# Kernel optimization log

Measured on AMD Instinct MI355X. Metric: run time of the kernel, lower is better.

Reference implementation:

```python
import jax, jax.numpy as jnp
import numpy as np

DIM = 512
HEADS = 8
EPS = 1e-3  # keras LayerNormalization default epsilon


def setup_inputs() -> dict:
    key = jax.random.key(0)
    ks = jax.random.split(key, 12)
    B, H, W, C = 8, 32, 32, DIM
    s = 0.02
    return {
        "x": jax.random.normal(ks[0], (B, H, W, C), jnp.float32),
        "ln_gamma": jnp.ones((C,), jnp.float32),
        "ln_beta": jnp.zeros((C,), jnp.float32),
        "qkv_d_w": jax.random.normal(ks[1], (C, 3 * C), jnp.float32) * s,
        "qkv_d_b": jnp.zeros((3 * C,), jnp.float32),
        "qkv_s_w": jax.random.normal(ks[2], (C, 3 * C), jnp.float32) * s,
        "qkv_s_b": jnp.zeros((3 * C,), jnp.float32),
        "proj_d_w": jax.random.normal(ks[3], (C, C), jnp.float32) * s,
        "proj_d_b": jnp.zeros((C,), jnp.float32),
        "proj_s_w": jax.random.normal(ks[4], (C, C), jnp.float32) * s,
        "proj_s_b": jnp.zeros((C,), jnp.float32),
        "fusion_weight": jnp.ones((2,), jnp.float32),
    }


def _split_heads(t, B, N):
    # [B, N, C] -> [B, heads, N, head_dim]
    return t.reshape(B, N, HEADS, -1).transpose(0, 2, 1, 3)


def _merge_heads(t, B, N, C):
    # [B, heads, N, head_dim] -> [B, N, C]
    return t.transpose(0, 2, 1, 3).reshape(B, N, C)


def reference(x, ln_gamma, ln_beta, qkv_d_w, qkv_d_b, qkv_s_w, qkv_s_b,
              proj_d_w, proj_d_b, proj_s_w, proj_s_b, fusion_weight):
    B, H, W, C = x.shape
    N = H * W
    scale = (C // HEADS) ** -0.5

    xf = x.reshape(B, N, C)
    mu = jnp.mean(xf, axis=-1, keepdims=True)
    var = jnp.var(xf, axis=-1, keepdims=True)
    xf = (xf - mu) * jax.lax.rsqrt(var + EPS) * ln_gamma + ln_beta

    # dense (softmax) branch
    qkv_d = xf @ qkv_d_w + qkv_d_b
    q_d, k_d, v_d = (
        _split_heads(t, B, N) for t in jnp.split(qkv_d, 3, axis=-1)
    )
    logits_d = jnp.einsum("bhnd,bhmd->bhnm", q_d, k_d) * scale
    out_d = jnp.einsum("bhnm,bhmd->bhnd", jax.nn.softmax(logits_d, axis=-1), v_d)
    out_d = _merge_heads(out_d, B, N, C) @ proj_d_w + proj_d_b

    # sparse (relu^2) branch
    qkv_s = xf @ qkv_s_w + qkv_s_b
    q_s, k_s, v_s = (
        _split_heads(t, B, N) for t in jnp.split(qkv_s, 3, axis=-1)
    )
    rq = jnp.square(jax.nn.relu(q_s))
    rk = jnp.square(jax.nn.relu(k_s))
    logits_s = jnp.einsum("bhnd,bhmd->bhnm", rq, rk) * scale
    out_s = jnp.einsum("bhnm,bhmd->bhnd", logits_s, v_s)
    out_s = _merge_heads(out_s, B, N, C) @ proj_s_w + proj_s_b

    alpha = jax.nn.softmax(fusion_weight)
    out = alpha[0] * out_s + alpha[1] * out_d
    return out.reshape(B, H, W, C)
```

## Files before the change

### kernel.cpp

```cpp
#include <hip/hip_runtime.h>
#include <math.h>

#define M_ROWS   8192
#define CDIM     512
#define QKV_N    1536
#define NTOK     1024
#define HEADS    8
#define HD       64
#define EPS      1e-3f
#define SCALE    0.125f

typedef __attribute__((ext_vector_type(8))) short short8;
typedef __attribute__((ext_vector_type(4))) float f32x4;
typedef unsigned short ushort_t;


__device__ __forceinline__ ushort_t f2bf(float f) {
    union { float f; unsigned int u; } v; v.f = f;
    unsigned int r = v.u + 0x7fffu + ((v.u >> 16) & 1u);
    return (ushort_t)(r >> 16);
}
__device__ __forceinline__ float bf2f(ushort_t u) {
    union { unsigned int u; float f; } v; v.u = ((unsigned int)u) << 16;
    return v.f;
}

__device__ __forceinline__ void get_alpha(const float* __restrict__ fw,
                                          float& a0, float& a1)
{
    const float m  = fmaxf(fw[0], fw[1]);
    const float e0 = __expf(fw[0] - m);
    const float e1 = __expf(fw[1] - m);
    const float inv = 1.0f / (e0 + e1);
    a0 = e0 * inv;
    a1 = e1 * inv;
}


__global__ __launch_bounds__(256) void ln_kernel(const float* __restrict__ x,
                                                 const float* __restrict__ gamma,
                                                 const float* __restrict__ beta,
                                                 ushort_t* __restrict__ xhi,
                                                 ushort_t* __restrict__ xlo)
{
    const int row = blockIdx.x;
    const int t   = threadIdx.x;
    const float2 v = ((const float2*)(x + (size_t)row * CDIM))[t];
    float s  = v.x + v.y;
    float ss = v.x * v.x + v.y * v.y;
#pragma unroll
    for (int off = 32; off > 0; off >>= 1) {
        s  += __shfl_xor(s,  off, 64);
        ss += __shfl_xor(ss, off, 64);
    }
    __shared__ float red[8];
    __shared__ float stats[2];
    const int wid = t >> 6, lane = t & 63;
    if (lane == 0) { red[wid] = s; red[4 + wid] = ss; }
    __syncthreads();
    if (t == 0) {
        const float S  = red[0] + red[1] + red[2] + red[3];
        const float SS = red[4] + red[5] + red[6] + red[7];
        const float mu  = S * (1.0f / CDIM);
        const float var = SS * (1.0f / CDIM) - mu * mu;
        stats[0] = mu;
        stats[1] = rsqrtf(var + EPS);
    }
    __syncthreads();
    const float mu = stats[0], rs = stats[1];
    const float2 gv = ((const float2*)gamma)[t];
    const float2 bv = ((const float2*)beta)[t];
    const float ox = (v.x - mu) * rs * gv.x + bv.x;
    const float oy = (v.y - mu) * rs * gv.y + bv.y;
    ushort2 h2, l2;
    h2.x = f2bf(ox); l2.x = f2bf(ox - bf2f(h2.x));
    h2.y = f2bf(oy); l2.y = f2bf(oy - bf2f(h2.y));
    ((ushort2*)(xhi + (size_t)row * CDIM))[t] = h2;
    ((ushort2*)(xlo + (size_t)row * CDIM))[t] = l2;
}


__global__ __launch_bounds__(256) void tconv_kernel(const float* __restrict__ W,
                                                    ushort_t* __restrict__ hiT,
                                                    ushort_t* __restrict__ loT,
                                                    int N, int ors, int coff)
{
    const int t  = threadIdx.x;
    const int bk = blockIdx.x * 64, bn = blockIdx.y * 64;
    __shared__ float tile[64][65];
#pragma unroll
    for (int i = 0; i < 4; ++i) {
        const int idx = t + i * 256;
        const int kl = idx >> 4, nl = (idx & 15) * 4;
        const float4 v = *(const float4*)(W + (size_t)(bk + kl) * N + bn + nl);
        tile[kl][nl] = v.x; tile[kl][nl + 1] = v.y;
        tile[kl][nl + 2] = v.z; tile[kl][nl + 3] = v.w;
    }
    __syncthreads();
#pragma unroll
    for (int i = 0; i < 2; ++i) {
        const int idx = t + i * 256;
        const int nl = idx >> 3, kc = (idx & 7) * 8;
        short8 hv, lv;
#pragma unroll
        for (int j = 0; j < 8; ++j) {
            const float f = tile[kc + j][nl];
            const ushort_t h = f2bf(f);
            hv[j] = (short)h;
            lv[j] = (short)f2bf(f - bf2f(h));
        }
        const size_t ob = (size_t)(bn + nl) * ors + coff + bk + kc;
        *(short8*)(hiT + ob) = hv;
        if (loT) *(short8*)(loT + ob) = lv;
    }
}


template<int SPLIT, int OUTBF>
__global__ __launch_bounds__(256) void gemm_bf16_mfma(const ushort_t* __restrict__ Ahi,
                                                      const ushort_t* __restrict__ Alo,
                                                      const ushort_t* __restrict__ Bhi,
                                                      const ushort_t* __restrict__ Blo,
                                                      const float* __restrict__ bias,
                                                      float* __restrict__ C,
                                                      ushort_t* __restrict__ Cb,
                                                      int N, int K)
{
    const int t  = threadIdx.x;
    const int l  = t & 63, w = t >> 6;
    const int wr = w >> 1, wc = w & 1;
    const int lr = l & 15, lg = l >> 4;
    const int bm = blockIdx.x * 128, bn = blockIdx.y * 128;

    __shared__ ushort_t As[SPLIT ? 2 : 1][128 * 64];
    __shared__ ushort_t Bs[SPLIT ? 2 : 1][128 * 64];

    f32x4 acc[4][4];
#pragma unroll
    for (int i = 0; i < 4; ++i)
#pragma unroll
        for (int j = 0; j < 4; ++j) acc[i][j] = (f32x4){0.f, 0.f, 0.f, 0.f};

    const int srow0  = t >> 3;
    const int schunk = t & 7;

    for (int kt = 0; kt < K; kt += 64) {
        __syncthreads();
#pragma unroll
        for (int i = 0; i < 4; ++i) {
            const int row = srow0 + i * 32;
            const int cs  = ((schunk ^ (row & 7)) * 8);
            const size_t ga = (size_t)(bm + row) * K + kt + schunk * 8;
            const size_t gb = (size_t)(bn + row) * K + kt + schunk * 8;
            *(short8*)(&As[0][row * 64 + cs]) = *(const short8*)(Ahi + ga);
            *(short8*)(&Bs[0][row * 64 + cs]) = *(const short8*)(Bhi + gb);
            if (SPLIT) {
                *(short8*)(&As[1][row * 64 + cs]) = *(const short8*)(Alo + ga);
                *(short8*)(&Bs[1][row * 64 + cs]) = *(const short8*)(Blo + gb);
            }
        }
        __syncthreads();
#pragma unroll
        for (int ks = 0; ks < 2; ++ks) {
            short8 ah[4], bh[4], al[4], bl[4];
#pragma unroll
            for (int mf = 0; mf < 4; ++mf) {
                const int row = wr * 64 + mf * 16 + lr;
                const int cs  = (((ks * 4 + lg) ^ (row & 7)) * 8);
                ah[mf] = *(const short8*)(&As[0][row * 64 + cs]);
                if (SPLIT) al[mf] = *(const short8*)(&As[1][row * 64 + cs]);
            }
#pragma unroll
            for (int nf = 0; nf < 4; ++nf) {
                const int row = wc * 64 + nf * 16 + lr;
                const int cs  = (((ks * 4 + lg) ^ (row & 7)) * 8);
                bh[nf] = *(const short8*)(&Bs[0][row * 64 + cs]);
                if (SPLIT) bl[nf] = *(const short8*)(&Bs[1][row * 64 + cs]);
            }
#pragma unroll
            for (int mf = 0; mf < 4; ++mf)
#pragma unroll
                for (int nf = 0; nf < 4; ++nf) {
                    acc[mf][nf] = __builtin_amdgcn_mfma_f32_16x16x32_bf16(ah[mf], bh[nf], acc[mf][nf], 0, 0, 0);
                    if (SPLIT) {
                        acc[mf][nf] = __builtin_amdgcn_mfma_f32_16x16x32_bf16(al[mf], bh[nf], acc[mf][nf], 0, 0, 0);
                        acc[mf][nf] = __builtin_amdgcn_mfma_f32_16x16x32_bf16(ah[mf], bl[nf], acc[mf][nf], 0, 0, 0);
                    }
                }
        }
    }
    float bv[4];
#pragma unroll
    for (int nf = 0; nf < 4; ++nf) bv[nf] = bias[bn + wc * 64 + nf * 16 + lr];
#pragma unroll
    for (int mf = 0; mf < 4; ++mf)
#pragma unroll
        for (int r = 0; r < 4; ++r) {
            const int row = bm + wr * 64 + mf * 16 + lg * 4 + r;
            if (OUTBF) {
                ushort_t* cp = Cb + (size_t)row * N + bn + wc * 64;
#pragma unroll
                for (int nf = 0; nf < 4; ++nf)
                    cp[nf * 16 + lr] = f2bf(acc[mf][nf][r] + bv[nf]);
            } else {
                float* cp = C + (size_t)row * N + bn + wc * 64;
#pragma unroll
                for (int nf = 0; nf < 4; ++nf)
                    cp[nf * 16 + lr] = acc[mf][nf][r] + bv[nf];
            }
        }
}


__global__ __launch_bounds__(256) void vt_kernel(const ushort_t* __restrict__ qkvd_bf,
                                                 ushort_t* __restrict__ vtg)
{
    const int t  = threadIdx.x;
    const int bh = blockIdx.x, nt = blockIdx.y;
    const int b  = bh >> 3, h = bh & 7;
    __shared__ ushort_t tile[64 * 72];
    const int row = t >> 2, c16 = (t & 3) * 16;
    const size_t src = (size_t)(b * NTOK + nt * 64 + row) * QKV_N + 2 * CDIM + h * HD + c16;
    *(short8*)(tile + row * 72 + c16)     = *(const short8*)(qkvd_bf + src);
    *(short8*)(tile + row * 72 + c16 + 8) = *(const short8*)(qkvd_bf + src + 8);
    __syncthreads();
    const int d = t >> 2, tc = (t & 3) * 16;
    short8 o0, o1;
#pragma unroll
    for (int i = 0; i < 8; ++i) {
        o0[i] = (short)tile[(tc + i) * 72 + d];
        o1[i] = (short)tile[(tc + 8 + i) * 72 + d];
    }
    const size_t dst = ((size_t)bh * 64 + d) * NTOK + nt * 64 + tc;
    *(short8*)(vtg + dst)     = o0;
    *(short8*)(vtg + dst + 8) = o1;
}


__global__ __launch_bounds__(256) void attn_dense_mfma(const ushort_t* __restrict__ qkvd_bf,
                                                       const ushort_t* __restrict__ vtg,
                                                       const float* __restrict__ fw,
                                                       ushort_t* __restrict__ athi,
                                                       ushort_t* __restrict__ atlo)
{
    const int t  = threadIdx.x;
    const int l  = t & 63;
    const int w  = t >> 6;
    const int lr = l & 15;
    const int lg = l >> 4;

    const int blk = blockIdx.x;
    const int xcd = blk & 7;
    const int ixl = blk >> 3;
    const int bh  = ((ixl >> 4) << 3) + xcd;
    const int qt  = ixl & 15;
    const int b   = bh >> 3, h = bh & 7;

    __shared__ ushort_t Qs[64 * 72];
    __shared__ ushort_t Ks[64 * 72];
    __shared__ ushort_t Vs[64 * 72];
    __shared__ ushort_t Ps[64 * 72];

    const int srow = t >> 2, sc = (t & 3) * 16;

    {
        const size_t src = (size_t)(b * NTOK + qt * 64 + srow) * QKV_N + h * HD + sc;
        *(short8*)(Qs + srow * 72 + sc)     = *(const short8*)(qkvd_bf + src);
        *(short8*)(Qs + srow * 72 + sc + 8) = *(const short8*)(qkvd_bf + src + 8);
    }
    __syncthreads();

    const short8 aQ0 = *(const short8*)(Qs + (w * 16 + lr) * 72 + lg * 8);
    const short8 aQ1 = *(const short8*)(Qs + (w * 16 + lr) * 72 + 32 + lg * 8);

    f32x4 oacc[4];
#pragma unroll
    for (int i = 0; i < 4; ++i) oacc[i] = (f32x4){0.f, 0.f, 0.f, 0.f};
    float lsum[4] = {0.f, 0.f, 0.f, 0.f};

    for (int kt2 = 0; kt2 < 16; ++kt2) {
        __syncthreads();
        {
            const size_t ksrc = (size_t)(b * NTOK + kt2 * 64 + srow) * QKV_N + CDIM + h * HD + sc;
            *(short8*)(Ks + srow * 72 + sc)     = *(const short8*)(qkvd_bf + ksrc);
            *(short8*)(Ks + srow * 72 + sc + 8) = *(const short8*)(qkvd_bf + ksrc + 8);
            const size_t vsrc = ((size_t)bh * 64 + srow) * NTOK + kt2 * 64 + sc;
            *(short8*)(Vs + srow * 72 + sc)     = *(const short8*)(vtg + vsrc);
            *(short8*)(Vs + srow * 72 + sc + 8) = *(const short8*)(vtg + vsrc + 8);
        }
        __syncthreads();

        f32x4 s[4];
#pragma unroll
        for (int nf = 0; nf < 4; ++nf) {
            const short8 b0 = *(const short8*)(Ks + (nf * 16 + lr) * 72 + lg * 8);
            const short8 b1 = *(const short8*)(Ks + (nf * 16 + lr) * 72 + 32 + lg * 8);
            f32x4 z = {0.f, 0.f, 0.f, 0.f};
            z = __builtin_amdgcn_mfma_f32_16x16x32_bf16(aQ0, b0, z, 0, 0, 0);
            z = __builtin_amdgcn_mfma_f32_16x16x32_bf16(aQ1, b1, z, 0, 0, 0);
            s[nf] = z;
        }

#pragma unroll
        for (int nf = 0; nf < 4; ++nf) {
#pragma unroll
            for (int r = 0; r < 4; ++r) {
                const float p = __expf(s[nf][r] * SCALE);
                lsum[r] += p;
                Ps[(w * 16 + lg * 4 + r) * 72 + nf * 16 + lr] = f2bf(p);
            }
        }
        __syncthreads();

        const short8 aP0 = *(const short8*)(Ps + (w * 16 + lr) * 72 + lg * 8);
        const short8 aP1 = *(const short8*)(Ps + (w * 16 + lr) * 72 + 32 + lg * 8);
#pragma unroll
        for (int nfd = 0; nfd < 4; ++nfd) {
            const short8 b0 = *(const short8*)(Vs + (nfd * 16 + lr) * 72 + lg * 8);
            const short8 b1 = *(const short8*)(Vs + (nfd * 16 + lr) * 72 + 32 + lg * 8);
            oacc[nfd] = __builtin_amdgcn_mfma_f32_16x16x32_bf16(aP0, b0, oacc[nfd], 0, 0, 0);
            oacc[nfd] = __builtin_amdgcn_mfma_f32_16x16x32_bf16(aP1, b1, oacc[nfd], 0, 0, 0);
        }
    }

#pragma unroll
    for (int r = 0; r < 4; ++r) {
        lsum[r] += __shfl_xor(lsum[r], 1, 64);
        lsum[r] += __shfl_xor(lsum[r], 2, 64);
        lsum[r] += __shfl_xor(lsum[r], 4, 64);
        lsum[r] += __shfl_xor(lsum[r], 8, 64);
    }
    float a0, a1;
    get_alpha(fw, a0, a1);
    const size_t obase = ((size_t)(b * NTOK + qt * 64)) * 1024 + CDIM + h * HD;
#pragma unroll
    for (int r = 0; r < 4; ++r) {
        const int qrow = w * 16 + lg * 4 + r;
        const float sc2 = a1 / lsum[r];
        const size_t orow = obase + (size_t)qrow * 1024;
#pragma unroll
        for (int nfd = 0; nfd < 4; ++nfd) {
            const float v = oacc[nfd][r] * sc2;
            const ushort_t hv = f2bf(v);
            athi[orow + nfd * 16 + lr] = hv;
            atlo[orow + nfd * 16 + lr] = f2bf(v - bf2f(hv));
        }
    }
}


__global__ __launch_bounds__(256) void sparse_kv_kernel(const float* __restrict__ qkvs,
                                                        float* __restrict__ kvpart)
{
    const int t     = threadIdx.x;
    const int bh    = blockIdx.x >> 2;
    const int chunk = blockIdx.x & 3;
    const int b     = bh >> 3, h = bh & 7;
    const int j     = t >> 2, g = t & 3;
    __shared__ __align__(16) float ks[64 * 68];
    __shared__ __align__(16) float vs[64 * 68];
    float4 acc[4];
#pragma unroll
    for (int c4 = 0; c4 < 4; ++c4) acc[c4] = make_float4(0.f, 0.f, 0.f, 0.f);

    const size_t bbase = (size_t)b * NTOK * QKV_N;
    for (int mt = chunk * 4; mt < chunk * 4 + 4; ++mt) {
        __syncthreads();
        {
            const float* ksrc = qkvs + bbase + (size_t)(mt * 64) * QKV_N + CDIM + h * HD;
            const float* vsrc = ksrc + CDIM;
#pragma unroll
            for (int i = 0; i < 4; ++i) {
                const int idx = t + i * 256;
                const int row = idx >> 4, c4 = (idx & 15) * 4;
                *(float4*)(ks + row * 68 + c4) = *(const float4*)(ksrc + (size_t)row * QKV_N + c4);
                *(float4*)(vs + row * 68 + c4) = *(const float4*)(vsrc + (size_t)row * QKV_N + c4);
            }
        }
        __syncthreads();
#pragma unroll 4
        for (int m = 0; m < 64; ++m) {
            const float kkv = ks[m * 68 + j];
            const float rk  = fmaxf(kkv, 0.f);
            const float rk2 = rk * rk;
#pragma unroll
            for (int c4 = 0; c4 < 4; ++c4) {
                const float4 vv = *(const float4*)(vs + m * 68 + g * 16 + c4 * 4);
                acc[c4].x += rk2 * vv.x; acc[c4].y += rk2 * vv.y;
                acc[c4].z += rk2 * vv.z; acc[c4].w += rk2 * vv.w;
            }
        }
    }
#pragma unroll
    for (int c4 = 0; c4 < 4; ++c4) {
        float4 w = acc[c4];
        w.x *= SCALE; w.y *= SCALE; w.z *= SCALE; w.w *= SCALE;
        *(float4*)(kvpart + ((size_t)blockIdx.x << 12) + j * 64 + g * 16 + c4 * 4) = w;
    }
}


__global__ __launch_bounds__(256) void sparse_out_kernel(const float* __restrict__ qkvs,
                                                         const float* __restrict__ kvpart,
                                                         const float* __restrict__ fw,
                                                         ushort_t* __restrict__ athi,
                                                         ushort_t* __restrict__ atlo)
{
    const int t   = threadIdx.x;
    const int blk = blockIdx.x;
    const int qt  = blk & 15;
    const int bh  = blk >> 4;
    const int b   = bh >> 3, h = bh & 7;
    const int r   = t >> 2, g = t & 3;
    __shared__ __align__(16) float qs[64 * 68];
    __shared__ __align__(16) float kvs[64 * 68];
    {
        const float* qsrc = qkvs + (size_t)b * NTOK * QKV_N + (size_t)(qt * 64) * QKV_N + h * HD;
        const float* p0 = kvpart + ((size_t)(bh * 4) << 12);
#pragma unroll
        for (int i = 0; i < 4; ++i) {
            const int idx = t + i * 256;
            const int row = idx >> 4, c4 = (idx & 15) * 4;
            *(float4*)(qs + row * 68 + c4) = *(const float4*)(qsrc + (size_t)row * QKV_N + c4);
            const int o = row * 64 + c4;
            float4 s0 = *(const float4*)(p0 + o);
            const float4 s1 = *(const float4*)(p0 + 4096 + o);
            const float4 s2 = *(const float4*)(p0 + 8192 + o);
            const float4 s3 = *(const float4*)(p0 + 12288 + o);
            s0.x += s1.x + s2.x + s3.x; s0.y += s1.y + s2.y + s3.y;
            s0.z += s1.z + s2.z + s3.z; s0.w += s1.w + s2.w + s3.w;
            *(float4*)(kvs + row * 68 + c4) = s0;
        }
    }
    __syncthreads();
    float4 acc[4];
#pragma unroll
    for (int c4 = 0; c4 < 4; ++c4) acc[c4] = make_float4(0.f, 0.f, 0.f, 0.f);
#pragma unroll 4
    for (int jj = 0; jj < 64; ++jj) {
        const float qv  = qs[r * 68 + jj];
        const float rq  = fmaxf(qv, 0.f);
        const float rq2 = rq * rq;
#pragma unroll
        for (int c4 = 0; c4 < 4; ++c4) {
            const float4 kvv = *(const float4*)(kvs + jj * 68 + g * 16 + c4 * 4);
            acc[c4].x += rq2 * kvv.x; acc[c4].y += rq2 * kvv.y;
            acc[c4].z += rq2 * kvv.z; acc[c4].w += rq2 * kvv.w;
        }
    }
    float a0, a1;
    get_alpha(fw, a0, a1);
    const size_t orow = ((size_t)(b * NTOK + qt * 64 + r)) * 1024 + h * HD;
#pragma unroll
    for (int c4 = 0; c4 < 4; ++c4) {
        float4 w = acc[c4];
        w.x *= a0; w.y *= a0; w.z *= a0; w.w *= a0;
        ushort4 hw, lw;
        hw.x = f2bf(w.x); lw.x = f2bf(w.x - bf2f(hw.x));
        hw.y = f2bf(w.y); lw.y = f2bf(w.y - bf2f(hw.y));
        hw.z = f2bf(w.z); lw.z = f2bf(w.z - bf2f(hw.z));
        hw.w = f2bf(w.w); lw.w = f2bf(w.w - bf2f(hw.w));
        *(ushort4*)(athi + orow + g * 16 + c4 * 4) = hw;
        *(ushort4*)(atlo + orow + g * 16 + c4 * 4) = lw;
    }
}


__global__ void bias_comb_kernel(const float* __restrict__ bs,
                                 const float* __restrict__ bd,
                                 const float* __restrict__ fw,
                                 float* __restrict__ out)
{
    float a0, a1;
    get_alpha(fw, a0, a1);
    const int t = threadIdx.x;
    out[t] = a0 * bs[t] + a1 * bd[t];
}


extern "C" void kernel_launch(void* const* d_in, const int* in_sizes, int n_in,
                              void* d_out, int out_size, void* d_ws, size_t ws_size,
                              hipStream_t stream)
{
    (void)in_sizes; (void)n_in; (void)out_size; (void)ws_size;

    const float* x        = (const float*)d_in[0];
    const float* ln_g     = (const float*)d_in[1];
    const float* ln_b     = (const float*)d_in[2];
    const float* qkv_d_w  = (const float*)d_in[3];
    const float* qkv_d_b  = (const float*)d_in[4];
    const float* qkv_s_w  = (const float*)d_in[5];
    const float* qkv_s_b  = (const float*)d_in[6];
    const float* proj_d_w = (const float*)d_in[7];
    const float* proj_d_b = (const float*)d_in[8];
    const float* proj_s_w = (const float*)d_in[9];
    const float* proj_s_b = (const float*)d_in[10];
    const float* fw       = (const float*)d_in[11];

    float* ws = (float*)d_ws;
    float*    qkvs    = ws;
    float*    kvpart  = ws + (size_t)12582912;
    float*    biasc   = ws + (size_t)13631488;
    ushort_t* qkvd_bf = (ushort_t*)(ws + (size_t)14680064);
    ushort_t* vtg     = (ushort_t*)(ws + (size_t)20971520);
    ushort_t* athi    = (ushort_t*)(ws + (size_t)23068672);
    ushort_t* atlo    = (ushort_t*)(ws + (size_t)27262976);
    ushort_t* xhi     = (ushort_t*)(ws + (size_t)31457280);
    ushort_t* xlo     = (ushort_t*)(ws + (size_t)33554432);
    ushort_t* WdT_hi  = (ushort_t*)(ws + (size_t)35651584);
    ushort_t* WsT_hi  = (ushort_t*)(ws + (size_t)36044800);
    ushort_t* WsT_lo  = (ushort_t*)(ws + (size_t)36438016);
    ushort_t* WpT_hi  = (ushort_t*)(ws + (size_t)36831232);
    ushort_t* WpT_lo  = (ushort_t*)(ws + (size_t)37093376);

    ln_kernel<<<8192, 256, 0, stream>>>(x, ln_g, ln_b, xhi, xlo);
    tconv_kernel<<<dim3(8, 24), 256, 0, stream>>>(qkv_d_w, WdT_hi, nullptr, QKV_N, CDIM, 0);
    tconv_kernel<<<dim3(8, 24), 256, 0, stream>>>(qkv_s_w, WsT_hi, WsT_lo, QKV_N, CDIM, 0);
    tconv_kernel<<<dim3(8, 8), 256, 0, stream>>>(proj_s_w, WpT_hi, WpT_lo, CDIM, 1024, 0);
    tconv_kernel<<<dim3(8, 8), 256, 0, stream>>>(proj_d_w, WpT_hi, WpT_lo, CDIM, 1024, 512);
    bias_comb_kernel<<<1, 512, 0, stream>>>(proj_s_b, proj_d_b, fw, biasc);

    gemm_bf16_mfma<0, 1><<<dim3(64, 12), 256, 0, stream>>>(xhi, nullptr, WdT_hi, nullptr,
                                                           qkv_d_b, nullptr, qkvd_bf, QKV_N, CDIM);
    gemm_bf16_mfma<1, 0><<<dim3(64, 12), 256, 0, stream>>>(xhi, xlo, WsT_hi, WsT_lo,
                                                           qkv_s_b, qkvs, nullptr, QKV_N, CDIM);

    vt_kernel<<<dim3(64, 16), 256, 0, stream>>>(qkvd_bf, vtg);
    attn_dense_mfma<<<1024, 256, 0, stream>>>(qkvd_bf, vtg, fw, athi, atlo);

    sparse_kv_kernel<<<256, 256, 0, stream>>>(qkvs, kvpart);
    sparse_out_kernel<<<1024, 256, 0, stream>>>(qkvs, kvpart, fw, athi, atlo);

    gemm_bf16_mfma<1, 0><<<dim3(64, 4), 256, 0, stream>>>(athi, atlo, WpT_hi, WpT_lo,
                                                          biasc, (float*)d_out, nullptr, CDIM, 1024);
}
```

Before: 212.3 us.

## Transpose dense attention MFMAs so P stays wave-local and drop a barrier

```diff
diff --git a/kernel.cpp b/kernel.cpp
--- a/kernel.cpp
+++ b/kernel.cpp
@@ -9,6 +9,7 @@
 #define HD       64
 #define EPS      1e-3f
 #define SCALE    0.125f
+#define SCL2E    0.18033688011112042f
 
 typedef __attribute__((ext_vector_type(8))) short short8;
 typedef __attribute__((ext_vector_type(4))) float f32x4;
@@ -259,7 +260,7 @@
     __shared__ ushort_t Qs[64 * 72];
     __shared__ ushort_t Ks[64 * 72];
     __shared__ ushort_t Vs[64 * 72];
-    __shared__ ushort_t Ps[64 * 72];
+    __shared__ ushort_t Pq[64 * 72];
 
     const int srow = t >> 2, sc = (t & 3) * 16;
 
@@ -270,13 +271,13 @@
     }
     __syncthreads();
 
-    const short8 aQ0 = *(const short8*)(Qs + (w * 16 + lr) * 72 + lg * 8);
-    const short8 aQ1 = *(const short8*)(Qs + (w * 16 + lr) * 72 + 32 + lg * 8);
+    const short8 bQ0 = *(const short8*)(Qs + (w * 16 + lr) * 72 + lg * 8);
+    const short8 bQ1 = *(const short8*)(Qs + (w * 16 + lr) * 72 + 32 + lg * 8);
 
     f32x4 oacc[4];
 #pragma unroll
     for (int i = 0; i < 4; ++i) oacc[i] = (f32x4){0.f, 0.f, 0.f, 0.f};
-    float lsum[4] = {0.f, 0.f, 0.f, 0.f};
+    float lsum = 0.f;
 
     for (int kt2 = 0; kt2 < 16; ++kt2) {
         __syncthreads();
@@ -290,61 +291,54 @@
         }
         __syncthreads();
 
-        f32x4 s[4];
-#pragma unroll
-        for (int nf = 0; nf < 4; ++nf) {
-            const short8 b0 = *(const short8*)(Ks + (nf * 16 + lr) * 72 + lg * 8);
-            const short8 b1 = *(const short8*)(Ks + (nf * 16 + lr) * 72 + 32 + lg * 8);
+#pragma unroll
+        for (int kb = 0; kb < 4; ++kb) {
+            const short8 aK0 = *(const short8*)(Ks + (kb * 16 + lr) * 72 + lg * 8);
+            const short8 aK1 = *(const short8*)(Ks + (kb * 16 + lr) * 72 + 32 + lg * 8);
             f32x4 z = {0.f, 0.f, 0.f, 0.f};
-            z = __builtin_amdgcn_mfma_f32_16x16x32_bf16(aQ0, b0, z, 0, 0, 0);
-            z = __builtin_amdgcn_mfma_f32_16x16x32_bf16(aQ1, b1, z, 0, 0, 0);
-            s[nf] = z;
-        }
-
-#pragma unroll
-        for (int nf = 0; nf < 4; ++nf) {
-#pragma unroll
-            for (int r = 0; r < 4; ++r) {
-                const float p = __expf(s[nf][r] * SCALE);
-                lsum[r] += p;
-                Ps[(w * 16 + lg * 4 + r) * 72 + nf * 16 + lr] = f2bf(p);
-            }
-        }
-        __syncthreads();
-
-        const short8 aP0 = *(const short8*)(Ps + (w * 16 + lr) * 72 + lg * 8);
-        const short8 aP1 = *(const short8*)(Ps + (w * 16 + lr) * 72 + 32 + lg * 8);
+            z = __builtin_amdgcn_mfma_f32_16x16x32_bf16(aK0, bQ0, z, 0, 0, 0);
+            z = __builtin_amdgcn_mfma_f32_16x16x32_bf16(aK1, bQ1, z, 0, 0, 0);
+            const float p0 = exp2f(z[0] * SCL2E);
+            const float p1 = exp2f(z[1] * SCL2E);
+            const float p2 = exp2f(z[2] * SCL2E);
+            const float p3 = exp2f(z[3] * SCL2E);
+            lsum += (p0 + p1) + (p2 + p3);
+            unsigned int r01, r23;
+            asm("v_cvt_pk_bf16_f32 %0, %1, %2" : "=v"(r01) : "v"(p0), "v"(p1));
+            asm("v_cvt_pk_bf16_f32 %0, %1, %2" : "=v"(r23) : "v"(p2), "v"(p3));
+            uint2 pw; pw.x = r01; pw.y = r23;
+            *(uint2*)(Pq + (w * 16 + lr) * 72 + kb * 16 + lg * 4) = pw;
+        }
+
+        const short8 bP0 = *(const short8*)(Pq + (w * 16 + lr) * 72 + lg * 8);
+        const short8 bP1 = *(const short8*)(Pq + (w * 16 + lr) * 72 + 32 + lg * 8);
 #pragma unroll
         for (int nfd = 0; nfd < 4; ++nfd) {
-            const short8 b0 = *(const short8*)(Vs + (nfd * 16 + lr) * 72 + lg * 8);
-            const short8 b1 = *(const short8*)(Vs + (nfd * 16 + lr) * 72 + 32 + lg * 8);
-            oacc[nfd] = __builtin_amdgcn_mfma_f32_16x16x32_bf16(aP0, b0, oacc[nfd], 0, 0, 0);
-            oacc[nfd] = __builtin_amdgcn_mfma_f32_16x16x32_bf16(aP1, b1, oacc[nfd], 0, 0, 0);
-        }
-    }
-
-#pragma unroll
-    for (int r = 0; r < 4; ++r) {
-        lsum[r] += __shfl_xor(lsum[r], 1, 64);
-        lsum[r] += __shfl_xor(lsum[r], 2, 64);
-        lsum[r] += __shfl_xor(lsum[r], 4, 64);
-        lsum[r] += __shfl_xor(lsum[r], 8, 64);
-    }
+            const short8 aV0 = *(const short8*)(Vs + (nfd * 16 + lr) * 72 + lg * 8);
+            const short8 aV1 = *(const short8*)(Vs + (nfd * 16 + lr) * 72 + 32 + lg * 8);
+            oacc[nfd] = __builtin_amdgcn_mfma_f32_16x16x32_bf16(aV0, bP0, oacc[nfd], 0, 0, 0);
+            oacc[nfd] = __builtin_amdgcn_mfma_f32_16x16x32_bf16(aV1, bP1, oacc[nfd], 0, 0, 0);
+        }
+    }
+
+    lsum += __shfl_xor(lsum, 16, 64);
+    lsum += __shfl_xor(lsum, 32, 64);
     float a0, a1;
     get_alpha(fw, a0, a1);
-    const size_t obase = ((size_t)(b * NTOK + qt * 64)) * 1024 + CDIM + h * HD;
-#pragma unroll
-    for (int r = 0; r < 4; ++r) {
-        const int qrow = w * 16 + lg * 4 + r;
-        const float sc2 = a1 / lsum[r];
-        const size_t orow = obase + (size_t)qrow * 1024;
-#pragma unroll
-        for (int nfd = 0; nfd < 4; ++nfd) {
+    const float sc2 = a1 / lsum;
+    const size_t orow = ((size_t)(b * NTOK + qt * 64 + w * 16 + lr)) * 1024 + CDIM + h * HD;
+#pragma unroll
+    for (int nfd = 0; nfd < 4; ++nfd) {
+        ushort4 hw, lw;
+#pragma unroll
+        for (int r = 0; r < 4; ++r) {
             const float v = oacc[nfd][r] * sc2;
             const ushort_t hv = f2bf(v);
-            athi[orow + nfd * 16 + lr] = hv;
-            atlo[orow + nfd * 16 + lr] = f2bf(v - bf2f(hv));
-        }
+            ((ushort_t*)&hw)[r] = hv;
+            ((ushort_t*)&lw)[r] = f2bf(v - bf2f(hv));
+        }
+        *(ushort4*)(athi + orow + nfd * 16 + lg * 4) = hw;
+        *(ushort4*)(atlo + orow + nfd * 16 + lg * 4) = lw;
     }
 }
 
```

New measurement: 210.7 us. About the same (-0.7%).
